# Kernel optimization log

Hardware: AMD Instinct MI355X
Metric: run time of the kernel (lower is better)

The kernel has to match this reference:

```python
import jax, jax.numpy as jnp
import numpy as np
jax.config.update("jax_enable_x64", True)

T, C, F = 2048, 2048, 8192
f32 = jnp.float32
f64 = jnp.float64


def setup_inputs() -> dict:
    key = jax.random.key(0)
    ks = jax.random.split(key, 20)
    s = 0.02
    return {
        "x": jax.random.normal(ks[0], (T, C), f32),
        "att_shift": jnp.zeros((C,), f32),
        "wkv_state": jnp.zeros((2, C), f32),
        "ffn_shift": jnp.zeros((C,), f32),
        "ln1_w": jnp.ones((C,), f32),
        "ln1_b": jnp.zeros((C,), f32),
        "ln2_w": jnp.ones((C,), f32),
        "ln2_b": jnp.zeros((C,), f32),
        "time_mix_k": jax.random.uniform(ks[1], (C,), f32),
        "time_mix_v": jax.random.uniform(ks[2], (C,), f32),
        "time_mix_r": jax.random.uniform(ks[3], (C,), f32),
        "time_decay": jax.random.normal(ks[4], (C,), f32) * 0.5,
        "time_first": jax.random.normal(ks[5], (C,), f32) * 0.5,
        "att_key": jax.random.normal(ks[6], (C, C), f32) * s,
        "att_value": jax.random.normal(ks[7], (C, C), f32) * s,
        "att_receptance": jax.random.normal(ks[8], (C, C), f32) * s,
        "att_output": jax.random.normal(ks[9], (C, C), f32) * s,
        "ffn_time_mix_k": jax.random.uniform(ks[10], (C,), f32),
        "ffn_time_mix_r": jax.random.uniform(ks[11], (C,), f32),
        "ffn_key": jax.random.normal(ks[12], (F, C), f32) * s,
        "ffn_value": jax.random.normal(ks[13], (C, F), f32) * s,
        "ffn_receptance": jax.random.normal(ks[14], (C, C), f32) * s,
    }


def _ln(x, w, b):
    m = x.mean(-1, keepdims=True)
    v = x.var(-1, keepdims=True)
    return (x - m) * jax.lax.rsqrt(v + 1e-5) * w + b


def _wkv(time_decay, time_first, k, v, wkv_state):
    # faithful to wkv_mop: double-precision math, float32 state round-trip per step
    u = time_first.astype(f64)
    w = -jnp.exp(time_decay.astype(f64))
    ew = jnp.exp(w)

    def step(carry, kv_t):
        a, b = carry  # float32 states [C]
        k_t, v_t = kv_t
        kd = k_t.astype(f64)
        vd = v_t.astype(f64)
        e = jnp.exp(u + w + kd)
        y = (a + e * vd) / (b + e)
        kk = jnp.exp(kd)
        a2 = ((a + kk * vd) * ew).astype(f32)
        b2 = ((b + kk) * ew).astype(f32)
        return (a2, b2), y.astype(f32)

    _, y = jax.lax.scan(step, (wkv_state[0], wkv_state[1]), (k, v))
    return y  # [T, C]


def reference(x, att_shift, wkv_state, ffn_shift, ln1_w, ln1_b, ln2_w, ln2_b,
              time_mix_k, time_mix_v, time_mix_r, time_decay, time_first,
              att_key, att_value, att_receptance, att_output,
              ffn_time_mix_k, ffn_time_mix_r, ffn_key, ffn_value, ffn_receptance):
    # --- TimeMix (att) on rx = ln1(x); shiftamount=2 -> prev token of rx ---
    rx = _ln(x, ln1_w, ln1_b)                         # [T, C]
    xx = jnp.concatenate([att_shift[None, :], rx[:-1]], axis=0)
    xk = rx * time_mix_k + xx * (1.0 - time_mix_k)
    xv = rx * time_mix_v + xx * (1.0 - time_mix_v)
    xr = rx * time_mix_r + xx * (1.0 - time_mix_r)
    k = xk @ att_key.T                                # [T, C]
    v = xv @ att_value.T
    sr = jax.nn.sigmoid(xr @ att_receptance.T)
    y = _wkv(time_decay, time_first, k, v, wkv_state)
    x = x + (sr * y) @ att_output.T
    # --- ChannelMix (ffn) on fx = ln2(x); shift = prev token of fx ---
    fx = _ln(x, ln2_w, ln2_b)
    fxx = jnp.concatenate([ffn_shift[None, :], fx[:-1]], axis=0)
    fk = fx * ffn_time_mix_k + fxx * (1.0 - ffn_time_mix_k)
    fr = fx * ffn_time_mix_r + fxx * (1.0 - ffn_time_mix_r)
    kf = jnp.square(jax.nn.relu(fk @ ffn_key.T))      # [T, F]
    kv = kf @ ffn_value.T                             # [T, C]
    out = x + jax.nn.sigmoid(fr @ ffn_receptance.T) * kv
    return out
```

## Files before the change

kernel.cpp:

```cpp
#include <hip/hip_runtime.h>
#include <hip/hip_bf16.h>

typedef unsigned short u16;
typedef short bf16x8 __attribute__((ext_vector_type(8)));
typedef float f32x4 __attribute__((ext_vector_type(4)));

#define T_DIM 2048
#define C_DIM 2048
#define F_DIM 8192
#define WKV_L 32
#define WKV_P (T_DIM / WKV_L)

__device__ __forceinline__ u16 f2bf(float f) {
    unsigned int u = __float_as_uint(f);
    u += 0x7fff + ((u >> 16) & 1);
    return (u16)(u >> 16);
}

__device__ __forceinline__ void async16(const void* g, void* l) {
    __builtin_amdgcn_global_load_lds(
        (__attribute__((address_space(1))) const unsigned int*)g,
        (__attribute__((address_space(3))) unsigned int*)l, 16, 0, 0);
}

__global__ __launch_bounds__(256) void ln_mix3(
        const float* __restrict__ x, const float* __restrict__ sh,
        const float* __restrict__ w, const float* __restrict__ b,
        const float* __restrict__ mk, const float* __restrict__ mv,
        const float* __restrict__ mr,
        u16* __restrict__ xk, u16* __restrict__ xv, u16* __restrict__ xr) {
    __shared__ float red[16];
    const int t = blockIdx.x, tid = threadIdx.x;
    const float4* cr = (const float4*)(x + (size_t)t * C_DIM);
    float4 c0 = cr[tid * 2], c1 = cr[tid * 2 + 1];
    float s = c0.x + c0.y + c0.z + c0.w + c1.x + c1.y + c1.z + c1.w;
    float q = c0.x * c0.x + c0.y * c0.y + c0.z * c0.z + c0.w * c0.w
            + c1.x * c1.x + c1.y * c1.y + c1.z * c1.z + c1.w * c1.w;
    float4 p0, p1;
    float sp = 0.f, qp = 0.f;
    if (t > 0) {
        const float4* pr = (const float4*)(x + (size_t)(t - 1) * C_DIM);
        p0 = pr[tid * 2]; p1 = pr[tid * 2 + 1];
        sp = p0.x + p0.y + p0.z + p0.w + p1.x + p1.y + p1.z + p1.w;
        qp = p0.x * p0.x + p0.y * p0.y + p0.z * p0.z + p0.w * p0.w
           + p1.x * p1.x + p1.y * p1.y + p1.z * p1.z + p1.w * p1.w;
    } else {
        const float4* pr = (const float4*)sh;
        p0 = pr[tid * 2]; p1 = pr[tid * 2 + 1];
    }
    #pragma unroll
    for (int off = 32; off > 0; off >>= 1) {
        s += __shfl_down(s, off);   q += __shfl_down(q, off);
        sp += __shfl_down(sp, off); qp += __shfl_down(qp, off);
    }
    const int lane = tid & 63, wv = tid >> 6;
    if (lane == 0) { red[wv] = s; red[4 + wv] = q; red[8 + wv] = sp; red[12 + wv] = qp; }
    __syncthreads();
    if (tid == 0) {
        red[0] += red[1] + red[2] + red[3];
        red[4] += red[5] + red[6] + red[7];
        red[8] += red[9] + red[10] + red[11];
        red[12] += red[13] + red[14] + red[15];
    }
    __syncthreads();
    const float mc = red[0] * (1.f / C_DIM);
    const float ic = rsqrtf(red[4] * (1.f / C_DIM) - mc * mc + 1e-5f);
    const float mp = red[8] * (1.f / C_DIM);
    const float ip = rsqrtf(red[12] * (1.f / C_DIM) - mp * mp + 1e-5f);
    const float4* w4 = (const float4*)w;
    const float4* b4 = (const float4*)b;
    #pragma unroll
    for (int j = 0; j < 2; ++j) {
        const int i4 = tid * 2 + j;
        float4 cv = j ? c1 : c0, pv = j ? p1 : p0;
        float4 wv4 = w4[i4], bv = b4[i4];
        float4 cl, pl;
        cl.x = (cv.x - mc) * ic * wv4.x + bv.x;
        cl.y = (cv.y - mc) * ic * wv4.y + bv.y;
        cl.z = (cv.z - mc) * ic * wv4.z + bv.z;
        cl.w = (cv.w - mc) * ic * wv4.w + bv.w;
        if (t > 0) {
            pl.x = (pv.x - mp) * ip * wv4.x + bv.x;
            pl.y = (pv.y - mp) * ip * wv4.y + bv.y;
            pl.z = (pv.z - mp) * ip * wv4.z + bv.z;
            pl.w = (pv.w - mp) * ip * wv4.w + bv.w;
        } else pl = pv;
        const size_t o = (size_t)t * (C_DIM / 4) + i4;
        float4 m;
        ushort4 r;
        m = ((const float4*)mk)[i4];
        r.x = f2bf(cl.x * m.x + pl.x * (1.f - m.x));
        r.y = f2bf(cl.y * m.y + pl.y * (1.f - m.y));
        r.z = f2bf(cl.z * m.z + pl.z * (1.f - m.z));
        r.w = f2bf(cl.w * m.w + pl.w * (1.f - m.w));
        ((ushort4*)xk)[o] = r;
        m = ((const float4*)mv)[i4];
        r.x = f2bf(cl.x * m.x + pl.x * (1.f - m.x));
        r.y = f2bf(cl.y * m.y + pl.y * (1.f - m.y));
        r.z = f2bf(cl.z * m.z + pl.z * (1.f - m.z));
        r.w = f2bf(cl.w * m.w + pl.w * (1.f - m.w));
        ((ushort4*)xv)[o] = r;
        m = ((const float4*)mr)[i4];
        r.x = f2bf(cl.x * m.x + pl.x * (1.f - m.x));
        r.y = f2bf(cl.y * m.y + pl.y * (1.f - m.y));
        r.z = f2bf(cl.z * m.z + pl.z * (1.f - m.z));
        r.w = f2bf(cl.w * m.w + pl.w * (1.f - m.w));
        ((ushort4*)xr)[o] = r;
    }
}

__global__ __launch_bounds__(256) void ln_mix2(
        const float* __restrict__ x, const float* __restrict__ sh,
        const float* __restrict__ w, const float* __restrict__ b,
        const float* __restrict__ mk, const float* __restrict__ mr,
        u16* __restrict__ fk, u16* __restrict__ fr) {
    __shared__ float red[16];
    const int t = blockIdx.x, tid = threadIdx.x;
    const float4* cr = (const float4*)(x + (size_t)t * C_DIM);
    float4 c0 = cr[tid * 2], c1 = cr[tid * 2 + 1];
    float s = c0.x + c0.y + c0.z + c0.w + c1.x + c1.y + c1.z + c1.w;
    float q = c0.x * c0.x + c0.y * c0.y + c0.z * c0.z + c0.w * c0.w
            + c1.x * c1.x + c1.y * c1.y + c1.z * c1.z + c1.w * c1.w;
    float4 p0, p1;
    float sp = 0.f, qp = 0.f;
    if (t > 0) {
        const float4* pr = (const float4*)(x + (size_t)(t - 1) * C_DIM);
        p0 = pr[tid * 2]; p1 = pr[tid * 2 + 1];
        sp = p0.x + p0.y + p0.z + p0.w + p1.x + p1.y + p1.z + p1.w;
        qp = p0.x * p0.x + p0.y * p0.y + p0.z * p0.z + p0.w * p0.w
           + p1.x * p1.x + p1.y * p1.y + p1.z * p1.z + p1.w * p1.w;
    } else {
        const float4* pr = (const float4*)sh;
        p0 = pr[tid * 2]; p1 = pr[tid * 2 + 1];
    }
    #pragma unroll
    for (int off = 32; off > 0; off >>= 1) {
        s += __shfl_down(s, off);   q += __shfl_down(q, off);
        sp += __shfl_down(sp, off); qp += __shfl_down(qp, off);
    }
    const int lane = tid & 63, wv = tid >> 6;
    if (lane == 0) { red[wv] = s; red[4 + wv] = q; red[8 + wv] = sp; red[12 + wv] = qp; }
    __syncthreads();
    if (tid == 0) {
        red[0] += red[1] + red[2] + red[3];
        red[4] += red[5] + red[6] + red[7];
        red[8] += red[9] + red[10] + red[11];
        red[12] += red[13] + red[14] + red[15];
    }
    __syncthreads();
    const float mc = red[0] * (1.f / C_DIM);
    const float ic = rsqrtf(red[4] * (1.f / C_DIM) - mc * mc + 1e-5f);
    const float mp = red[8] * (1.f / C_DIM);
    const float ip = rsqrtf(red[12] * (1.f / C_DIM) - mp * mp + 1e-5f);
    const float4* w4 = (const float4*)w;
    const float4* b4 = (const float4*)b;
    #pragma unroll
    for (int j = 0; j < 2; ++j) {
        const int i4 = tid * 2 + j;
        float4 cv = j ? c1 : c0, pv = j ? p1 : p0;
        float4 wv4 = w4[i4], bv = b4[i4];
        float4 cl, pl;
        cl.x = (cv.x - mc) * ic * wv4.x + bv.x;
        cl.y = (cv.y - mc) * ic * wv4.y + bv.y;
        cl.z = (cv.z - mc) * ic * wv4.z + bv.z;
        cl.w = (cv.w - mc) * ic * wv4.w + bv.w;
        if (t > 0) {
            pl.x = (pv.x - mp) * ip * wv4.x + bv.x;
            pl.y = (pv.y - mp) * ip * wv4.y + bv.y;
            pl.z = (pv.z - mp) * ip * wv4.z + bv.z;
            pl.w = (pv.w - mp) * ip * wv4.w + bv.w;
        } else pl = pv;
        const size_t o = (size_t)t * (C_DIM / 4) + i4;
        float4 m;
        ushort4 r;
        m = ((const float4*)mk)[i4];
        r.x = f2bf(cl.x * m.x + pl.x * (1.f - m.x));
        r.y = f2bf(cl.y * m.y + pl.y * (1.f - m.y));
        r.z = f2bf(cl.z * m.z + pl.z * (1.f - m.z));
        r.w = f2bf(cl.w * m.w + pl.w * (1.f - m.w));
        ((ushort4*)fk)[o] = r;
        m = ((const float4*)mr)[i4];
        r.x = f2bf(cl.x * m.x + pl.x * (1.f - m.x));
        r.y = f2bf(cl.y * m.y + pl.y * (1.f - m.y));
        r.z = f2bf(cl.z * m.z + pl.z * (1.f - m.z));
        r.w = f2bf(cl.w * m.w + pl.w * (1.f - m.w));
        ((ushort4*)fr)[o] = r;
    }
}

__global__ __launch_bounds__(256) void cvt_bf16(const float* __restrict__ in,
                                                u16* __restrict__ out, int n8) {
    int i = blockIdx.x * 256 + threadIdx.x;
    const int stride = gridDim.x * 256;
    for (; i < n8; i += stride) {
        const float4* p = (const float4*)(in + (size_t)i * 8);
        float4 a = p[0], b = p[1];
        ushort4 lo, hi;
        lo.x = f2bf(a.x); lo.y = f2bf(a.y); lo.z = f2bf(a.z); lo.w = f2bf(a.w);
        hi.x = f2bf(b.x); hi.y = f2bf(b.y); hi.z = f2bf(b.z); hi.w = f2bf(b.w);
        ((ushort4*)out)[i * 2] = lo;
        ((ushort4*)out)[i * 2 + 1] = hi;
    }
}

__global__ __launch_bounds__(256) void cvt3_bf16(const float* __restrict__ i0,
                                                 const float* __restrict__ i1,
                                                 const float* __restrict__ i2,
                                                 u16* __restrict__ out, int n8) {
    const int sel = blockIdx.y;
    const float* in = sel == 0 ? i0 : (sel == 1 ? i1 : i2);
    u16* o = out + (size_t)sel * n8 * 8;
    int i = blockIdx.x * 256 + threadIdx.x;
    const int stride = gridDim.x * 256;
    for (; i < n8; i += stride) {
        const float4* p = (const float4*)(in + (size_t)i * 8);
        float4 a = p[0], b = p[1];
        ushort4 lo, hi;
        lo.x = f2bf(a.x); lo.y = f2bf(a.y); lo.z = f2bf(a.z); lo.w = f2bf(a.w);
        hi.x = f2bf(b.x); hi.y = f2bf(b.y); hi.z = f2bf(b.z); hi.w = f2bf(b.w);
        ((ushort4*)o)[i * 2] = lo;
        ((ushort4*)o)[i * 2 + 1] = hi;
    }
}

__global__ __launch_bounds__(256) void reduce4(const float* __restrict__ p0,
                                               const float* __restrict__ p1,
                                               const float* __restrict__ p2,
                                               const float* __restrict__ p3,
                                               float* __restrict__ o, int n4) {
    int i = blockIdx.x * 256 + threadIdx.x;
    const int stride = gridDim.x * 256;
    for (; i < n4; i += stride) {
        float4 a = ((const float4*)p0)[i], b = ((const float4*)p1)[i];
        float4 c = ((const float4*)p2)[i], d = ((const float4*)p3)[i];
        float4 r;
        r.x = a.x + b.x + c.x + d.x;
        r.y = a.y + b.y + c.y + d.y;
        r.z = a.z + b.z + c.z + d.z;
        r.w = a.w + b.w + c.w + d.w;
        ((float4*)o)[i] = r;
    }
}

__global__ __launch_bounds__(256) void wkv_part(const float* __restrict__ td,
                                                const float* __restrict__ k,
                                                const float* __restrict__ v,
                                                float* __restrict__ Ab,
                                                float* __restrict__ Bb) {
    const int idx = blockIdx.x * 256 + threadIdx.x;
    const int c = idx & (C_DIM - 1);
    const int p = idx >> 11;
    const float ew = expf(-expf(td[c]));
    float A = 0.f, B = 0.f;
    size_t o = (size_t)(p * WKV_L) * C_DIM + c;
    #pragma unroll 4
    for (int i = 0; i < WKV_L; ++i, o += C_DIM) {
        const float kk = expf(k[o]);
        A = (A + kk * v[o]) * ew;
        B = (B + kk) * ew;
    }
    Ab[p * C_DIM + c] = A;
    Bb[p * C_DIM + c] = B;
}

__global__ __launch_bounds__(256) void wkv_comb(const float* __restrict__ td,
                                                const float* __restrict__ st,
                                                const float* __restrict__ Ab,
                                                const float* __restrict__ Bb,
                                                float* __restrict__ Sa,
                                                float* __restrict__ Sb) {
    const int c = blockIdx.x * 256 + threadIdx.x;
    const float w = -expf(td[c]);
    const float dL = expf(w * (float)WKV_L);
    float a = st[c];
    float b = st[C_DIM + c];
    #pragma unroll 4
    for (int p = 0; p < WKV_P; ++p) {
        Sa[p * C_DIM + c] = a;
        Sb[p * C_DIM + c] = b;
        a = dL * a + Ab[p * C_DIM + c];
        b = dL * b + Bb[p * C_DIM + c];
    }
}

__global__ __launch_bounds__(256) void wkv_emit(const float* __restrict__ td,
                                                const float* __restrict__ tf,
                                                const float* __restrict__ k,
                                                const float* __restrict__ v,
                                                const float* __restrict__ r,
                                                const float* __restrict__ Sa,
                                                const float* __restrict__ Sb,
                                                u16* __restrict__ pout) {
    const int idx = blockIdx.x * 256 + threadIdx.x;
    const int c = idx & (C_DIM - 1);
    const int p = idx >> 11;
    const float u = tf[c];
    const float w = -expf(td[c]);
    const float ew = expf(w);
    float a = Sa[p * C_DIM + c];
    float b = Sb[p * C_DIM + c];
    size_t o = (size_t)(p * WKV_L) * C_DIM + c;
    #pragma unroll 2
    for (int i = 0; i < WKV_L; ++i, o += C_DIM) {
        const float kt = k[o], vt = v[o], rt = r[o];
        const float e = expf(u + w + kt);
        const float y = (a + e * vt) / (b + e);
        const float kk = expf(kt);
        a = (a + kk * vt) * ew;
        b = (b + kk) * ew;
        const float sr = 1.f / (1.f + expf(-rt));
        pout[o] = f2bf(sr * y);
    }
}

enum { EPI_F32 = 0, EPI_ADDX = 1, EPI_RELU2 = 2, EPI_SIGMULADD = 3 };

template <int EPI>
__global__ __launch_bounds__(512, 2) void gemm256(
        const u16* __restrict__ A, int lda, long a_zs,
        const u16* __restrict__ B, int ldb, long b_zs,
        int Kloop,
        void* __restrict__ outp, int ldo, long o_zs,
        const float* __restrict__ aux1, const float* __restrict__ aux2) {
    __shared__ u16 lds[4 * 16384];
    const int tid = threadIdx.x;
    const int l = tid & 63, w = tid >> 6;
    const int wr = w >> 2, wcn = w & 3;

    const int gx = gridDim.x, gy = gridDim.y;
    const int nxy = gx * gy;
    const int flat = (blockIdx.z * gy + blockIdx.y) * gx + blockIdx.x;
    const int cpx = (nxy * gridDim.z) >> 3;
    const int swz = (flat & 7) * cpx + (flat >> 3);
    const int z = swz / nxy;
    const int rem = swz - z * nxy;
    const int bm = rem % gy;
    const int bn = rem / gy;

    const u16* Ag = A + (size_t)z * a_zs + (size_t)bm * 256 * lda;
    const u16* Bg = B + (size_t)z * b_zs + (size_t)bn * 256 * ldb;

    long gA[2], gB[2];
    int dA[2], dB[2];
    #pragma unroll
    for (int j = 0; j < 2; ++j) {
        const int off = j * 8192 + w * 1024 + l * 16;
        const int row = off >> 6;
        const int cb = (off & 63) ^ (((off >> 9) & 1) << 5);
        gA[j] = (long)row * lda + (cb >> 1);
        gB[j] = (long)row * ldb + (cb >> 1);
        dA[j] = j * 4096 + w * 512;
        dB[j] = 8192 + j * 4096 + w * 512;
    }

    int offA[8], offB[4];
    #pragma unroll
    for (int m = 0; m < 8; ++m) {
        const int lin = (wr * 128 + m * 16 + (l & 15)) * 64 + ((l >> 4) << 4);
        offA[m] = (lin ^ (((lin >> 9) & 1) << 5)) >> 1;
    }
    #pragma unroll
    for (int n = 0; n < 4; ++n) {
        const int lin = (wcn * 64 + n * 16 + (l & 15)) * 64 + ((l >> 4) << 4);
        offB[n] = 8192 + ((lin ^ (((lin >> 9) & 1) << 5)) >> 1);
    }

    const f32x4 fz = {0.f, 0.f, 0.f, 0.f};
    f32x4 acc[8][4];
    #pragma unroll
    for (int m = 0; m < 8; ++m)
        #pragma unroll
        for (int n = 0; n < 4; ++n) acc[m][n] = fz;

    const int NT = Kloop >> 5;

    auto stage = [&](int kt, int sp) {
        const long ko = (long)kt << 5;
        const int sb = sp * 16384;
        async16(Ag + gA[0] + ko, &lds[sb + dA[0]]);
        async16(Ag + gA[1] + ko, &lds[sb + dA[1]]);
        async16(Bg + gB[0] + ko, &lds[sb + dB[0]]);
        async16(Bg + gB[1] + ko, &lds[sb + dB[1]]);
    };

    stage(0, 0);
    stage(1, 1);
    stage(2, 2);

    for (int t = 0; t < NT; ++t) {
        asm volatile("s_waitcnt vmcnt(8)" ::: "memory");
        __builtin_amdgcn_s_barrier();
        __builtin_amdgcn_sched_barrier(0);
        {
            const int tp = (t + 3 < NT) ? t + 3 : NT - 1;
            stage(tp, (t + 3) & 3);
        }
        const int sb = (t & 3) * 16384;
        bf16x8 af[8], bfv[4];
        #pragma unroll
        for (int m = 0; m < 8; ++m) af[m] = *(const bf16x8*)&lds[sb + offA[m]];
        #pragma unroll
        for (int n = 0; n < 4; ++n) bfv[n] = *(const bf16x8*)&lds[sb + offB[n]];
        __builtin_amdgcn_s_setprio(1);
        #pragma unroll
        for (int m = 0; m < 4; ++m)
            #pragma unroll
            for (int n = 0; n < 4; ++n)
                acc[m][n] = __builtin_amdgcn_mfma_f32_16x16x32_bf16(af[m], bfv[n], acc[m][n], 0, 0, 0);
        __builtin_amdgcn_s_setprio(0);
        __builtin_amdgcn_s_setprio(1);
        #pragma unroll
        for (int m = 4; m < 8; ++m)
            #pragma unroll
            for (int n = 0; n < 4; ++n)
                acc[m][n] = __builtin_amdgcn_mfma_f32_16x16x32_bf16(af[m], bfv[n], acc[m][n], 0, 0, 0);
        __builtin_amdgcn_s_setprio(0);
    }
    asm volatile("s_waitcnt vmcnt(0)" ::: "memory");

    const int r00 = bm * 256 + wr * 128 + ((l >> 4) << 2);
    const int c00 = bn * 256 + wcn * 64 + (l & 15);
    #pragma unroll
    for (int m = 0; m < 8; ++m) {
        #pragma unroll
        for (int n = 0; n < 4; ++n) {
            #pragma unroll
            for (int j = 0; j < 4; ++j) {
                const int rr = r00 + m * 16 + j;
                const int cc = c00 + n * 16;
                const size_t o = (size_t)rr * ldo + cc;
                const float val = acc[m][n][j];
                if constexpr (EPI == EPI_F32) {
                    ((float*)outp)[(size_t)z * o_zs + o] = val;
                } else {
                    const float tp2 = fmaxf(val, 0.f);
                    ((u16*)outp)[o] = f2bf(tp2 * tp2);
                }
            }
        }
    }
}

template <int EPI>
__global__ __launch_bounds__(256) void gemm_bt(const u16* __restrict__ A,
                                               const u16* __restrict__ B,
                                               int M, int N, int K,
                                               void* __restrict__ outp,
                                               const float* __restrict__ aux1,
                                               const float* __restrict__ aux2) {
    __shared__ u16 As[128 * 64];
    __shared__ u16 Bs[128 * 64];
    const int tid = threadIdx.x;
    const int lane = tid & 63, wid = tid >> 6;
    const int wr = wid >> 1, wc = wid & 1;
    const int bm = blockIdx.y, bn = blockIdx.x;

    const u16* Ag = A + (size_t)bm * 128 * K;
    const u16* Bg = B + (size_t)bn * 128 * K;

    const f32x4 fz = {0.f, 0.f, 0.f, 0.f};
    f32x4 acc[4][4];
    #pragma unroll
    for (int m = 0; m < 4; ++m)
        #pragma unroll
        for (int n = 0; n < 4; ++n) acc[m][n] = fz;

    const int nk = K >> 6;
    for (int kt = 0; kt < nk; ++kt) {
        const u16* Agk = Ag + (kt << 6);
        const u16* Bgk = Bg + (kt << 6);
        #pragma unroll
        for (int i = 0; i < 4; ++i) {
            const int id = i * 256 + tid;
            async16(Agk + (size_t)(id >> 3) * K + ((id & 7) << 3), &As[(i * 4 + wid) << 9]);
        }
        #pragma unroll
        for (int i = 0; i < 4; ++i) {
            const int id = i * 256 + tid;
            async16(Bgk + (size_t)(id >> 3) * K + ((id & 7) << 3), &Bs[(i * 4 + wid) << 9]);
        }
        __syncthreads();
        #pragma unroll
        for (int kk = 0; kk < 2; ++kk) {
            const int ko = (kk << 5) + ((lane >> 4) << 3);
            bf16x8 af[4], bfr[4];
            #pragma unroll
            for (int m = 0; m < 4; ++m)
                af[m] = *(const bf16x8*)&As[((wr << 6) + (m << 4) + (lane & 15)) * 64 + ko];
            #pragma unroll
            for (int n = 0; n < 4; ++n)
                bfr[n] = *(const bf16x8*)&Bs[((wc << 6) + (n << 4) + (lane & 15)) * 64 + ko];
            #pragma unroll
            for (int m = 0; m < 4; ++m)
                #pragma unroll
                for (int n = 0; n < 4; ++n)
                    acc[m][n] = __builtin_amdgcn_mfma_f32_16x16x32_bf16(af[m], bfr[n], acc[m][n], 0, 0, 0);
        }
        __syncthreads();
    }

    const int r0 = bm * 128 + (wr << 6) + ((lane >> 4) << 2);
    const int c0 = bn * 128 + (wc << 6) + (lane & 15);
    #pragma unroll
    for (int m = 0; m < 4; ++m) {
        #pragma unroll
        for (int n = 0; n < 4; ++n) {
            #pragma unroll
            for (int j = 0; j < 4; ++j) {
                const int rr = r0 + (m << 4) + j;
                const int cc = c0 + (n << 4);
                const size_t o = (size_t)rr * N + cc;
                const float val = acc[m][n][j];
                if constexpr (EPI == EPI_ADDX) {
                    ((float*)outp)[o] = aux1[o] + val;
                } else {
                    const float sg = 1.f / (1.f + expf(-val));
                    ((float*)outp)[o] = aux1[o] + sg * aux2[o];
                }
            }
        }
    }
}

extern "C" void kernel_launch(void* const* d_in, const int* in_sizes, int n_in,
                              void* d_out, int out_size, void* d_ws, size_t ws_size,
                              hipStream_t stream) {
    const float* x         = (const float*)d_in[0];
    const float* att_shift = (const float*)d_in[1];
    const float* wkv_state = (const float*)d_in[2];
    const float* ffn_shift = (const float*)d_in[3];
    const float* ln1w = (const float*)d_in[4];
    const float* ln1b = (const float*)d_in[5];
    const float* ln2w = (const float*)d_in[6];
    const float* ln2b = (const float*)d_in[7];
    const float* tmk  = (const float*)d_in[8];
    const float* tmv  = (const float*)d_in[9];
    const float* tmr  = (const float*)d_in[10];
    const float* td   = (const float*)d_in[11];
    const float* tf   = (const float*)d_in[12];
    const float* Wk   = (const float*)d_in[13];
    const float* Wv   = (const float*)d_in[14];
    const float* Wr   = (const float*)d_in[15];
    const float* Wo   = (const float*)d_in[16];
    const float* ftmk = (const float*)d_in[17];
    const float* ftmr = (const float*)d_in[18];
    const float* Wfk  = (const float*)d_in[19];
    const float* Wfv  = (const float*)d_in[20];
    const float* Wfr  = (const float*)d_in[21];
    float* out = (float*)d_out;

    char* ws = (char*)d_ws;
    const size_t MB = 1ull << 20;
    float* rx0 = (float*)(ws + 0);
    u16*   xk  = (u16*)(ws + 16 * MB);
    u16*   xv  = (u16*)(ws + 24 * MB);
    u16*   xr  = (u16*)(ws + 32 * MB);
    float* kb  = (float*)(ws + 40 * MB);
    float* vb  = (float*)(ws + 56 * MB);
    float* rb  = (float*)(ws + 72 * MB);
    u16*   pb  = (u16*)(ws + 88 * MB);
    float* x1  = (float*)(ws + 96 * MB);
    u16*   kf  = (u16*)(ws + 112 * MB);
    u16*   Wb  = (u16*)(ws + 144 * MB);
    float* wAb = (float*)(ws + 112 * MB);
    float* wBb = (float*)(ws + 112 * MB + 512 * 1024);
    float* wSa = (float*)(ws + 113 * MB);
    float* wSb = (float*)(ws + 113 * MB + 512 * 1024);
    float* fvp = (float*)(ws + 32 * MB);

    const int T = T_DIM, C = C_DIM, F = F_DIM;
    const dim3 blk(256), blk5(512);

    ln_mix3<<<T, blk, 0, stream>>>(x, att_shift, ln1w, ln1b, tmk, tmv, tmr, xk, xv, xr);

    cvt3_bf16<<<dim3(1024, 3), blk, 0, stream>>>(Wk, Wv, Wr, Wb, C * C / 8);
    gemm256<EPI_F32><<<dim3(C / 256, T / 256, 3), blk5, 0, stream>>>(
        xk, C, (long)T * C, Wb, C, (long)C * C, C, kb, C, (long)T * C, nullptr, nullptr);

    wkv_part<<<(C * WKV_P) / 256, blk, 0, stream>>>(td, kb, vb, wAb, wBb);
    wkv_comb<<<C / 256, blk, 0, stream>>>(td, wkv_state, wAb, wBb, wSa, wSb);
    wkv_emit<<<(C * WKV_P) / 256, blk, 0, stream>>>(td, tf, kb, vb, rb, wSa, wSb, pb);

    cvt_bf16<<<2048, blk, 0, stream>>>(Wo, Wb, C * C / 8);
    gemm_bt<EPI_ADDX><<<dim3(C / 128, T / 128), blk, 0, stream>>>(
        pb, Wb, T, C, C, x1, x, nullptr);

    ln_mix2<<<T, blk, 0, stream>>>(x1, ffn_shift, ln2w, ln2b, ftmk, ftmr, xk, xv);

    cvt_bf16<<<2048, blk, 0, stream>>>(Wfk, Wb, F * C / 8);
    gemm256<EPI_RELU2><<<dim3(F / 256, T / 256, 1), blk5, 0, stream>>>(
        xk, C, 0, Wb, C, 0, C, kf, F, 0, nullptr, nullptr);

    cvt_bf16<<<2048, blk, 0, stream>>>(Wfv, Wb, C * F / 8);
    gemm256<EPI_F32><<<dim3(C / 256, T / 256, 4), blk5, 0, stream>>>(
        kf, F, 2048, Wb, F, 2048, 2048, fvp, C, (long)T * C, nullptr, nullptr);
    reduce4<<<2048, blk, 0, stream>>>(fvp, fvp + (size_t)T * C, fvp + 2 * (size_t)T * C,
                                      fvp + 3 * (size_t)T * C, rx0, T * C / 4);

    cvt_bf16<<<2048, blk, 0, stream>>>(Wfr, Wb, C * C / 8);
    gemm_bt<EPI_SIGMULADD><<<dim3(C / 128, T / 128), blk, 0, stream>>>(
        xv, Wb, T, C, C, out, x1, rx0);
}
```

Before: 421.8 us.

## Swap big GEMMs to 128-tile kernel and split-K small GEMMs with separate epilogues

Generalizes gemm_bt with strides, z-batching, a split-K offset and a swizzled block order. The QKV and FFN-key GEMMs now use the 128x128 kernel instead of the 256x256 one. The output and receptance projections are split-K by two, with the residual add and sigmoid epilogues moved into new elementwise combine kernels. The aim is more blocks per GEMM for better CU occupancy, at the cost of extra fp32 partial writes and reads and extra kernel launches.

```diff
diff --git a/kernel.cpp b/kernel.cpp
--- a/kernel.cpp
+++ b/kernel.cpp
@@ -242,6 +242,43 @@
     }
 }
 
+__global__ __launch_bounds__(256) void comb_add(const float* __restrict__ p0,
+                                                const float* __restrict__ p1,
+                                                const float* __restrict__ xin,
+                                                float* __restrict__ o, int n4) {
+    int i = blockIdx.x * 256 + threadIdx.x;
+    const int stride = gridDim.x * 256;
+    for (; i < n4; i += stride) {
+        float4 a = ((const float4*)p0)[i], b = ((const float4*)p1)[i];
+        float4 c = ((const float4*)xin)[i];
+        float4 r;
+        r.x = a.x + b.x + c.x;
+        r.y = a.y + b.y + c.y;
+        r.z = a.z + b.z + c.z;
+        r.w = a.w + b.w + c.w;
+        ((float4*)o)[i] = r;
+    }
+}
+
+__global__ __launch_bounds__(256) void comb_sig(const float* __restrict__ p0,
+                                                const float* __restrict__ p1,
+                                                const float* __restrict__ x1,
+                                                const float* __restrict__ kv,
+                                                float* __restrict__ o, int n4) {
+    int i = blockIdx.x * 256 + threadIdx.x;
+    const int stride = gridDim.x * 256;
+    for (; i < n4; i += stride) {
+        float4 a = ((const float4*)p0)[i], b = ((const float4*)p1)[i];
+        float4 c = ((const float4*)x1)[i], d = ((const float4*)kv)[i];
+        float4 r;
+        r.x = c.x + d.x / (1.f + expf(-(a.x + b.x)));
+        r.y = c.y + d.y / (1.f + expf(-(a.y + b.y)));
+        r.z = c.z + d.z / (1.f + expf(-(a.z + b.z)));
+        r.w = c.w + d.w / (1.f + expf(-(a.w + b.w)));
+        ((float4*)o)[i] = r;
+    }
+}
+
 __global__ __launch_bounds__(256) void wkv_part(const float* __restrict__ td,
                                                 const float* __restrict__ k,
                                                 const float* __restrict__ v,
@@ -313,7 +350,7 @@
     }
 }
 
-enum { EPI_F32 = 0, EPI_ADDX = 1, EPI_RELU2 = 2, EPI_SIGMULADD = 3 };
+enum { EPI_F32 = 0, EPI_RELU2 = 2 };
 
 template <int EPI>
 __global__ __launch_bounds__(512, 2) void gemm256(
@@ -442,21 +479,30 @@
 }
 
 template <int EPI>
-__global__ __launch_bounds__(256) void gemm_bt(const u16* __restrict__ A,
-                                               const u16* __restrict__ B,
-                                               int M, int N, int K,
-                                               void* __restrict__ outp,
-                                               const float* __restrict__ aux1,
-                                               const float* __restrict__ aux2) {
+__global__ __launch_bounds__(256) void gemm_bt(
+        const u16* __restrict__ A, int lda, long a_zs,
+        const u16* __restrict__ B, int ldb, long b_zs,
+        long koff, int Kloop,
+        void* __restrict__ outp, int ldo, long o_zs,
+        const float* __restrict__ aux1) {
     __shared__ u16 As[128 * 64];
     __shared__ u16 Bs[128 * 64];
     const int tid = threadIdx.x;
     const int lane = tid & 63, wid = tid >> 6;
-    const int wr = wid >> 1, wc = wid & 1;
-    const int bm = blockIdx.y, bn = blockIdx.x;
-
-    const u16* Ag = A + (size_t)bm * 128 * K;
-    const u16* Bg = B + (size_t)bn * 128 * K;
+    const int wr2 = wid >> 1, wc2 = wid & 1;
+
+    const int gx = gridDim.x, gy = gridDim.y;
+    const int nxy = gx * gy;
+    const int flat = (blockIdx.z * gy + blockIdx.y) * gx + blockIdx.x;
+    const int cpx = (nxy * gridDim.z) >> 3;
+    const int swz = (flat & 7) * cpx + (flat >> 3);
+    const int z = swz / nxy;
+    const int rem = swz - z * nxy;
+    const int bm = rem % gy;
+    const int bn = rem / gy;
+
+    const u16* Ag = A + (size_t)z * a_zs + (size_t)z * koff + (size_t)bm * 128 * lda;
+    const u16* Bg = B + (size_t)z * b_zs + (size_t)z * koff + (size_t)bn * 128 * ldb;
 
     const f32x4 fz = {0.f, 0.f, 0.f, 0.f};
     f32x4 acc[4][4];
@@ -465,19 +511,19 @@
         #pragma unroll
         for (int n = 0; n < 4; ++n) acc[m][n] = fz;
 
-    const int nk = K >> 6;
+    const int nk = Kloop >> 6;
     for (int kt = 0; kt < nk; ++kt) {
         const u16* Agk = Ag + (kt << 6);
         const u16* Bgk = Bg + (kt << 6);
         #pragma unroll
         for (int i = 0; i < 4; ++i) {
             const int id = i * 256 + tid;
-            async16(Agk + (size_t)(id >> 3) * K + ((id & 7) << 3), &As[(i * 4 + wid) << 9]);
+            async16(Agk + (size_t)(id >> 3) * lda + ((id & 7) << 3), &As[(i * 4 + wid) << 9]);
         }
         #pragma unroll
         for (int i = 0; i < 4; ++i) {
             const int id = i * 256 + tid;
-            async16(Bgk + (size_t)(id >> 3) * K + ((id & 7) << 3), &Bs[(i * 4 + wid) << 9]);
+            async16(Bgk + (size_t)(id >> 3) * ldb + ((id & 7) << 3), &Bs[(i * 4 + wid) << 9]);
         }
         __syncthreads();
         #pragma unroll
@@ -486,10 +532,10 @@
             bf16x8 af[4], bfr[4];
             #pragma unroll
             for (int m = 0; m < 4; ++m)
-                af[m] = *(const bf16x8*)&As[((wr << 6) + (m << 4) + (lane & 15)) * 64 + ko];
+                af[m] = *(const bf16x8*)&As[((wr2 << 6) + (m << 4) + (lane & 15)) * 64 + ko];
             #pragma unroll
             for (int n = 0; n < 4; ++n)
-                bfr[n] = *(const bf16x8*)&Bs[((wc << 6) + (n << 4) + (lane & 15)) * 64 + ko];
+                bfr[n] = *(const bf16x8*)&Bs[((wc2 << 6) + (n << 4) + (lane & 15)) * 64 + ko];
             #pragma unroll
             for (int m = 0; m < 4; ++m)
                 #pragma unroll
@@ -499,8 +545,8 @@
         __syncthreads();
     }
 
-    const int r0 = bm * 128 + (wr << 6) + ((lane >> 4) << 2);
-    const int c0 = bn * 128 + (wc << 6) + (lane & 15);
+    const int r0 = bm * 128 + (wr2 << 6) + ((lane >> 4) << 2);
+    const int c0 = bn * 128 + (wc2 << 6) + (lane & 15);
     #pragma unroll
     for (int m = 0; m < 4; ++m) {
         #pragma unroll
@@ -509,13 +555,13 @@
             for (int j = 0; j < 4; ++j) {
                 const int rr = r0 + (m << 4) + j;
                 const int cc = c0 + (n << 4);
-                const size_t o = (size_t)rr * N + cc;
+                const size_t o = (size_t)z * o_zs + (size_t)rr * ldo + cc;
                 const float val = acc[m][n][j];
-                if constexpr (EPI == EPI_ADDX) {
-                    ((float*)outp)[o] = aux1[o] + val;
+                if constexpr (EPI == EPI_F32) {
+                    ((float*)outp)[o] = val;
                 } else {
-                    const float sg = 1.f / (1.f + expf(-val));
-                    ((float*)outp)[o] = aux1[o] + sg * aux2[o];
+                    const float tp2 = fmaxf(val, 0.f);
+                    ((u16*)outp)[o] = f2bf(tp2 * tp2);
                 }
             }
         }
@@ -566,7 +612,9 @@
     float* wBb = (float*)(ws + 112 * MB + 512 * 1024);
     float* wSa = (float*)(ws + 113 * MB);
     float* wSb = (float*)(ws + 113 * MB + 512 * 1024);
+    float* aop = (float*)(ws + 40 * MB);
     float* fvp = (float*)(ws + 32 * MB);
+    float* rcp = (float*)(ws + 32 * MB);
 
     const int T = T_DIM, C = C_DIM, F = F_DIM;
     const dim3 blk(256), blk5(512);
@@ -574,22 +622,23 @@
     ln_mix3<<<T, blk, 0, stream>>>(x, att_shift, ln1w, ln1b, tmk, tmv, tmr, xk, xv, xr);
 
     cvt3_bf16<<<dim3(1024, 3), blk, 0, stream>>>(Wk, Wv, Wr, Wb, C * C / 8);
-    gemm256<EPI_F32><<<dim3(C / 256, T / 256, 3), blk5, 0, stream>>>(
-        xk, C, (long)T * C, Wb, C, (long)C * C, C, kb, C, (long)T * C, nullptr, nullptr);
+    gemm_bt<EPI_F32><<<dim3(C / 128, T / 128, 3), blk, 0, stream>>>(
+        xk, C, (long)T * C, Wb, C, (long)C * C, 0, C, kb, C, (long)T * C, nullptr);
 
     wkv_part<<<(C * WKV_P) / 256, blk, 0, stream>>>(td, kb, vb, wAb, wBb);
     wkv_comb<<<C / 256, blk, 0, stream>>>(td, wkv_state, wAb, wBb, wSa, wSb);
     wkv_emit<<<(C * WKV_P) / 256, blk, 0, stream>>>(td, tf, kb, vb, rb, wSa, wSb, pb);
 
     cvt_bf16<<<2048, blk, 0, stream>>>(Wo, Wb, C * C / 8);
-    gemm_bt<EPI_ADDX><<<dim3(C / 128, T / 128), blk, 0, stream>>>(
-        pb, Wb, T, C, C, x1, x, nullptr);
+    gemm_bt<EPI_F32><<<dim3(C / 128, T / 128, 2), blk, 0, stream>>>(
+        pb, C, 0, Wb, C, 0, 1024, 1024, aop, C, (long)T * C, nullptr);
+    comb_add<<<2048, blk, 0, stream>>>(aop, aop + (size_t)T * C, x, x1, T * C / 4);
 
     ln_mix2<<<T, blk, 0, stream>>>(x1, ffn_shift, ln2w, ln2b, ftmk, ftmr, xk, xv);
 
     cvt_bf16<<<2048, blk, 0, stream>>>(Wfk, Wb, F * C / 8);
-    gemm256<EPI_RELU2><<<dim3(F / 256, T / 256, 1), blk5, 0, stream>>>(
-        xk, C, 0, Wb, C, 0, C, kf, F, 0, nullptr, nullptr);
+    gemm_bt<EPI_RELU2><<<dim3(F / 128, T / 128, 1), blk, 0, stream>>>(
+        xk, C, 0, Wb, C, 0, 0, C, kf, F, 0, nullptr);
 
     cvt_bf16<<<2048, blk, 0, stream>>>(Wfv, Wb, C * F / 8);
     gemm256<EPI_F32><<<dim3(C / 256, T / 256, 4), blk5, 0, stream>>>(
@@ -598,6 +647,7 @@
                                       fvp + 3 * (size_t)T * C, rx0, T * C / 4);
 
     cvt_bf16<<<2048, blk, 0, stream>>>(Wfr, Wb, C * C / 8);
-    gemm_bt<EPI_SIGMULADD><<<dim3(C / 128, T / 128), blk, 0, stream>>>(
-        xv, Wb, T, C, C, out, x1, rx0);
-}
+    gemm_bt<EPI_F32><<<dim3(C / 128, T / 128, 2), blk, 0, stream>>>(
+        xv, C, 0, Wb, C, 0, 1024, 1024, rcp, C, (long)T * C, nullptr);
+    comb_sig<<<2048, blk, 0, stream>>>(rcp, rcp + (size_t)T * C, x1, rx0, out, T * C / 4);
+}
```

Measured after the change: 485.8 us. 15.2% more time.
